# Kernel tuning notes

Hardware: AMD Instinct MI355X
Metric: run time of the kernel (lower is better)

The kernel has to match this reference:

```python
import jax, jax.numpy as jnp
import numpy as np

HEADS = 4
DIM_HEAD = 32
DIM = 256
EPS = 1e-12


def setup_inputs() -> dict:
    key = jax.random.key(0)
    ks = jax.random.split(key, 4)
    b, c, n = 8, DIM, 16384
    hidden = HEADS * DIM_HEAD  # 128
    x = jax.random.normal(ks[0], (b, c, n), dtype=jnp.float32)
    w_qkv = jax.random.normal(ks[1], (hidden * 3, c), dtype=jnp.float32) * (1.0 / np.sqrt(c))
    w_out = jax.random.normal(ks[2], (c, hidden), dtype=jnp.float32) * (1.0 / np.sqrt(hidden))
    b_out = jax.random.normal(ks[3], (c,), dtype=jnp.float32) * 0.01
    g = jnp.ones((1, c, 1), dtype=jnp.float32)
    return {"x": x, "w_qkv": w_qkv, "w_out": w_out, "b_out": b_out, "g": g}


def reference(x, w_qkv, w_out, b_out, g):
    b, c, n = x.shape
    scale = DIM_HEAD ** -0.5
    # to_qkv: Conv1d kernel-size 1, no bias == channel matmul
    qkv = jnp.einsum('oc,bcn->bon', w_qkv, x)  # [b, 3*h*d, n]
    q, k, v = jnp.split(qkv, 3, axis=1)
    def to_heads(t):
        return t.reshape(b, HEADS, DIM_HEAD, n)  # b (h d) n -> b h d n
    q, k, v = to_heads(q), to_heads(k), to_heads(v)
    q = jax.nn.softmax(q, axis=-2) * scale      # softmax over d
    k = jax.nn.softmax(k, axis=-1)              # softmax over n
    context = jnp.einsum('bhdn,bhen->bhde', k, v)  # [b,h,d,e]
    out = jnp.einsum('bhde,bhdn->bhen', context, q)  # [b,h,e,n]
    out = out.reshape(b, HEADS * DIM_HEAD, n)   # b h d n -> b (h d) n
    # to_out Conv1d (kernel 1) with bias
    out = jnp.einsum('oc,bcn->bon', w_out, out) + b_out[None, :, None]
    # RMSNorm: F.normalize over channel dim * g * sqrt(c)
    norm = jnp.sqrt(jnp.sum(out * out, axis=1, keepdims=True))
    out = out / jnp.maximum(norm, EPS) * g * jnp.sqrt(jnp.asarray(c, out.dtype))
    return out
```

## Files before the change

kernel.cpp:

```cpp
#include <hip/hip_runtime.h>
#include <hip/hip_bf16.h>
#include <math.h>

#define B_    8
#define C_    256
#define N_    16384
#define H_    4
#define D_    32
#define HID_  128
#define ROWS_ 384
#define SCALE 0.17677669529663687f

typedef __attribute__((ext_vector_type(8))) short bf16x8;
typedef __attribute__((ext_vector_type(16))) float f32x16;

__device__ __forceinline__ short f2bf(float f) {
    union { __hip_bfloat16 h; short s; } u;
    u.h = __float2bfloat16(f);
    return u.s;
}
__device__ __forceinline__ float bf2f(short s) {
    union { unsigned u; float f; } x;
    x.u = ((unsigned)(unsigned short)s) << 16;
    return x.f;
}

__global__ __launch_bounds__(256) void k_conv(
    const float* __restrict__ wqkv, const float* __restrict__ wout,
    short* __restrict__ wrearr, short* __restrict__ woutb)
{
    int i = blockIdx.x * 256 + threadIdx.x;
    if (i < 12288) {
        int tile = i >> 10;
        int ks   = (i >> 6) & 15;
        int l    = i & 63;
        int row  = tile * 32 + (l & 31);
        int k0   = ks * 16 + (l >> 5) * 8;
        const float* src = wqkv + row * 256 + k0;
        float4 f0 = *(const float4*)(src);
        float4 f1 = *(const float4*)(src + 4);
        short o[8] = {f2bf(f0.x), f2bf(f0.y), f2bf(f0.z), f2bf(f0.w),
                      f2bf(f1.x), f2bf(f1.y), f2bf(f1.z), f2bf(f1.w)};
        *(uint4*)(wrearr + (size_t)i * 8) = *(uint4*)o;
    } else {
        int j = (i - 12288) * 4;
        float4 f = *(const float4*)(wout + j);
        short4 s; s.x = f2bf(f.x); s.y = f2bf(f.y); s.z = f2bf(f.z); s.w = f2bf(f.w);
        *(short4*)(woutb + j) = s;
    }
}

__global__ __launch_bounds__(512, 2) void k_qkv(
    const float* __restrict__ x, const short* __restrict__ wrearr,
    short* __restrict__ qtb, short* __restrict__ part16,
    float* __restrict__ partden)
{
    __shared__ __align__(16) char  img[65536];
    __shared__ __align__(16) float xf[32 * 128];

    const int orig = blockIdx.x;
    const int swz  = (orig & 7) * 128 + (orig >> 3);
    const int b    = swz >> 7;
    const int nwin = swz & 127;
    const int nb   = nwin << 7;
    const int t    = threadIdx.x;
    const int l    = t & 63;
    const int wv   = t >> 6;
    const int h    = wv & 3;
    const int ch   = wv >> 2;
    const int c31  = l & 31;
    const int hf   = l >> 5;

    {
        const float* xg = x + (size_t)b * C_ * N_ + nb + (l & 31) * 4;
        const int cvn  = t & 127;
        const int cvkq = t >> 7;
        const float* xcol = xf + cvn;
        char* imgn = img + cvn * 512;
        const int swm = (cvn & 31) << 4;

        for (int c = 0; c < 8; c++) {
#pragma unroll
            for (int j = 0; j < 2; j++) {
                const int krow = (j * 8 + wv) * 2 + hf;
                const int kglob = c * 32 + krow;
                __builtin_amdgcn_global_load_lds(
                    (const __attribute__((address_space(1))) void*)(xg + (size_t)kglob * N_),
                    (__attribute__((address_space(3))) void*)((char*)xf + (j * 8 + wv) * 1024),
                    16, 0, 0);
            }
            __syncthreads();
#pragma unroll
            for (int p = 0; p < 4; p++) {
                const int kl = cvkq * 8 + p * 2;
                float f0 = xcol[(size_t)kl * 128];
                float f1 = xcol[(size_t)(kl + 1) * 128];
                const int kglob = c * 32 + kl;
                ushort2 v;
                v.x = (unsigned short)f2bf(f0);
                v.y = (unsigned short)f2bf(f1);
                *(ushort2*)(imgn + ((2 * kglob) ^ swm)) = v;
            }
            __syncthreads();
        }
    }

    f32x16 acc[3][2];
#pragma unroll
    for (int ti = 0; ti < 3; ti++)
#pragma unroll
        for (int ct = 0; ct < 2; ct++)
#pragma unroll
            for (int r = 0; r < 16; r++) acc[ti][ct][r] = 0.f;

    const bf16x8* wp = (const bf16x8*)wrearr + (size_t)h * 1024 + l;
    bf16x8 afN0 = wp[0], afN1 = wp[4096], afN2 = wp[8192];
    const char* smB0 = img + (ch * 64 + c31) * 512;
    const char* smB1 = img + (ch * 64 + 32 + c31) * 512;
#pragma unroll
    for (int ks = 0; ks < 16; ks++) {
        bf16x8 af0 = afN0, af1 = afN1, af2 = afN2;
        if (ks < 15) {
            afN0 = wp[(ks + 1) * 64];
            afN1 = wp[4096 + (ks + 1) * 64];
            afN2 = wp[8192 + (ks + 1) * 64];
        }
        const int slot = 2 * ks + hf;
        bf16x8 bfr0 = *(const bf16x8*)(smB0 + 16 * (slot ^ c31));
        bf16x8 bfr1 = *(const bf16x8*)(smB1 + 16 * (slot ^ c31));
        acc[0][0] = __builtin_amdgcn_mfma_f32_32x32x16_bf16(af0, bfr0, acc[0][0], 0, 0, 0);
        acc[0][1] = __builtin_amdgcn_mfma_f32_32x32x16_bf16(af0, bfr1, acc[0][1], 0, 0, 0);
        acc[1][0] = __builtin_amdgcn_mfma_f32_32x32x16_bf16(af1, bfr0, acc[1][0], 0, 0, 0);
        acc[1][1] = __builtin_amdgcn_mfma_f32_32x32x16_bf16(af1, bfr1, acc[1][1], 0, 0, 0);
        acc[2][0] = __builtin_amdgcn_mfma_f32_32x32x16_bf16(af2, bfr0, acc[2][0], 0, 0, 0);
        acc[2][1] = __builtin_amdgcn_mfma_f32_32x32x16_bf16(af2, bfr1, acc[2][1], 0, 0, 0);
    }


#pragma unroll
    for (int ct = 0; ct < 2; ct++) {
        float mx = -1e30f;
#pragma unroll
        for (int r = 0; r < 16; r++) mx = fmaxf(mx, acc[0][ct][r]);
        mx = fmaxf(mx, __shfl_xor(mx, 32));
        float e[16]; float s = 0.f;
#pragma unroll
        for (int r = 0; r < 16; r++) { e[r] = __expf(acc[0][ct][r] - mx); s += e[r]; }
        s += __shfl_xor(s, 32);
        float inv = SCALE / s;
        short* qp = qtb + ((size_t)b * HID_ + h * 32) * N_ + nb + ch * 64 + ct * 32 + c31;
#pragma unroll
        for (int r = 0; r < 16; r++) {
            int rm = (r & 3) + 8 * (r >> 2) + 4 * hf;
            qp[(size_t)rm * N_] = f2bf(e[r] * inv);
        }
    }
    __syncthreads();

    char* ekb = img + wv * 8192;
    char* vvb = ekb + 4096;
#pragma unroll
    for (int ct = 0; ct < 2; ct++)
#pragma unroll
        for (int r = 0; r < 16; r++) {
            int rm = (r & 3) + 8 * (r >> 2) + 4 * hf;
            int n  = ct * 32 + c31;
            int ad = rm * 128 + ((2 * n) ^ ((rm & 7) << 4));
            *(short*)(ekb + ad) = f2bf(__expf(acc[1][ct][r]));
            *(short*)(vvb + ad) = f2bf(acc[2][ct][r]);
        }

    f32x16 cD, dD;
#pragma unroll
    for (int r = 0; r < 16; r++) { cD[r] = 0.f; dD[r] = 0.f; }
    bf16x8 ones;
#pragma unroll
    for (int i = 0; i < 8; i++) ones[i] = (short)0x3F80;
#pragma unroll
    for (int ks = 0; ks < 4; ks++) {
        int slot = 2 * ks + hf;
        bf16x8 ea = *(const bf16x8*)(ekb + c31 * 128 + 16 * (slot ^ (c31 & 7)));
        bf16x8 vb = *(const bf16x8*)(vvb + c31 * 128 + 16 * (slot ^ (c31 & 7)));
        cD = __builtin_amdgcn_mfma_f32_32x32x16_bf16(ea, vb,   cD, 0, 0, 0);
        dD = __builtin_amdgcn_mfma_f32_32x32x16_bf16(ea, ones, dD, 0, 0, 0);
    }

    const int q64 = nwin * 2 + ch;
    short* pb = part16 + ((size_t)(b * 256 + q64) * 4 + h) * 1024;
#pragma unroll
    for (int r = 0; r < 16; r++) {
        int rm = (r & 3) + 8 * (r >> 2) + 4 * hf;
        pb[rm * 32 + c31] = f2bf(cD[r]);
    }
    if (c31 == 0) {
        float* pd = partden + ((size_t)(b * 256 + q64) * 4 + h) * 32;
#pragma unroll
        for (int r = 0; r < 16; r++) {
            int rm = (r & 3) + 8 * (r >> 2) + 4 * hf;
            pd[rm] = dD[r];
        }
    }
}

__global__ __launch_bounds__(256) void k_red(
    const short* __restrict__ part16, const float* __restrict__ partden,
    short* __restrict__ ctxbf)
{
    __shared__ float den_s[32];
    const int bh = blockIdx.x;
    const int b  = bh >> 2, h = bh & 3;
    const int t  = threadIdx.x;
    const int d  = t >> 3;
    const int e4 = (t & 7) * 4;

    const short* p0 = part16 + ((size_t)(b * 256) * 4 + h) * 1024 + d * 32 + e4;
    float s0 = 0.f, s1 = 0.f, s2 = 0.f, s3 = 0.f;
    for (int q = 0; q < 256; q++) {
        short4 v = *(const short4*)(p0 + (size_t)q * 4096);
        s0 += bf2f(v.x); s1 += bf2f(v.y); s2 += bf2f(v.z); s3 += bf2f(v.w);
    }
    if ((t & 7) == 0) {
        const float* pd = partden + ((size_t)(b * 256) * 4 + h) * 32 + d;
        float ds = 0.f;
        for (int q = 0; q < 256; q++) ds += pd[(size_t)q * 128];
        den_s[d] = ds;
    }
    __syncthreads();
    float inv = 1.0f / den_s[d];
    short* cb = ctxbf + (size_t)bh * 1024 + d;
    cb[(e4 + 0) * 32] = f2bf(s0 * inv);
    cb[(e4 + 1) * 32] = f2bf(s1 * inv);
    cb[(e4 + 2) * 32] = f2bf(s2 * inv);
    cb[(e4 + 3) * 32] = f2bf(s3 * inv);
}

__global__ __launch_bounds__(256, 3) void k_out(
    const short* __restrict__ qtb, const short* __restrict__ ctxbf,
    const short* __restrict__ woutb, const float* __restrict__ bout,
    const float* __restrict__ g, float* __restrict__ out)
{
    __shared__ __align__(16) char  hidS[16384];
    __shared__ float gl[C_], bl[C_];
    __shared__ float red[4][64];
    __shared__ float nrm[64];

    const int blk = blockIdx.x;
    const int b   = blk >> 8;
    const int n0  = (blk & 255) << 6;
    const int t   = threadIdx.x;
    const int l   = t & 63;
    const int wv  = t >> 6;
    const int c31 = l & 31;
    const int hf  = l >> 5;

    gl[t] = g[t];
    bl[t] = bout[t];
    __syncthreads();

    f32x16 hD[2];
#pragma unroll
    for (int ct = 0; ct < 2; ct++)
#pragma unroll
        for (int r = 0; r < 16; r++) hD[ct][r] = 0.f;
    const short* qb = qtb + (size_t)b * HID_ * N_ + n0;
    const short* cb = ctxbf + ((size_t)(b * H_ + wv) * 32 + c31) * 32;
#pragma unroll
    for (int ks = 0; ks < 2; ks++) {
        int k0 = ks * 16 + hf * 8;
        bf16x8 af = *(const bf16x8*)(cb + k0);
#pragma unroll
        for (int ct = 0; ct < 2; ct++) {
            bf16x8 bq;
#pragma unroll
            for (int i = 0; i < 8; i++)
                bq[i] = qb[(size_t)(wv * 32 + k0 + i) * N_ + ct * 32 + c31];
            hD[ct] = __builtin_amdgcn_mfma_f32_32x32x16_bf16(af, bq, hD[ct], 0, 0, 0);
        }
    }
#pragma unroll
    for (int ct = 0; ct < 2; ct++)
#pragma unroll
        for (int r = 0; r < 16; r++) {
            int rm = (r & 3) + 8 * (r >> 2) + 4 * hf;
            int hfull = wv * 32 + rm;
            int n = ct * 32 + c31;
            int ad = n * 256 + ((2 * hfull) ^ ((n & 15) << 4));
            *(short*)(hidS + ad) = f2bf(hD[ct][r]);
        }
    __syncthreads();

    f32x16 yacc[2][2];
#pragma unroll
    for (int rt = 0; rt < 2; rt++)
#pragma unroll
        for (int ct = 0; ct < 2; ct++)
#pragma unroll
            for (int r = 0; r < 16; r++) yacc[rt][ct][r] = 0.f;

#pragma unroll
    for (int ks = 0; ks < 8; ks++) {
        int k0 = ks * 16 + hf * 8;
        int sx = 2 * ks + hf;
        bf16x8 bq0 = *(const bf16x8*)(hidS + (c31)      * 256 + 16 * (sx ^ (c31 & 15)));
        bf16x8 bq1 = *(const bf16x8*)(hidS + (c31 + 32) * 256 + 16 * (sx ^ (c31 & 15)));
#pragma unroll
        for (int rt = 0; rt < 2; rt++) {
            bf16x8 af = *(const bf16x8*)(woutb + (wv * 64 + rt * 32 + c31) * HID_ + k0);
            yacc[rt][0] = __builtin_amdgcn_mfma_f32_32x32x16_bf16(af, bq0, yacc[rt][0], 0, 0, 0);
            yacc[rt][1] = __builtin_amdgcn_mfma_f32_32x32x16_bf16(af, bq1, yacc[rt][1], 0, 0, 0);
        }
    }

#pragma unroll
    for (int rt = 0; rt < 2; rt++)
#pragma unroll
        for (int r = 0; r < 16; r++) {
            int rm = (r & 3) + 8 * (r >> 2) + 4 * hf;
            float bo = bl[wv * 64 + rt * 32 + rm];
            yacc[rt][0][r] += bo;
            yacc[rt][1][r] += bo;
        }
#pragma unroll
    for (int ct = 0; ct < 2; ct++) {
        float s = 0.f;
#pragma unroll
        for (int rt = 0; rt < 2; rt++)
#pragma unroll
            for (int r = 0; r < 16; r++) s = fmaf(yacc[rt][ct][r], yacc[rt][ct][r], s);
        s += __shfl_xor(s, 32);
        if (hf == 0) red[wv][ct * 32 + c31] = s;
    }
    __syncthreads();
    if (t < 64) {
        float S = red[0][t] + red[1][t] + red[2][t] + red[3][t];
        nrm[t] = 16.0f / fmaxf(sqrtf(S), 1e-12f);
    }
    __syncthreads();

    float* ob = out + (size_t)b * C_ * N_ + n0;
#pragma unroll
    for (int rt = 0; rt < 2; rt++)
#pragma unroll
        for (int r = 0; r < 16; r++) {
            int rm = (r & 3) + 8 * (r >> 2) + 4 * hf;
            int c  = wv * 64 + rt * 32 + rm;
            float gc = gl[c];
#pragma unroll
            for (int ct = 0; ct < 2; ct++) {
                int n = ct * 32 + c31;
                __builtin_nontemporal_store(yacc[rt][ct][r] * gc * nrm[n],
                                            &ob[(size_t)c * N_ + n]);
            }
        }
}

extern "C" void kernel_launch(void* const* d_in, const int* in_sizes, int n_in,
                              void* d_out, int out_size, void* d_ws, size_t ws_size,
                              hipStream_t stream)
{
    const float* x    = (const float*)d_in[0];
    const float* wqkv = (const float*)d_in[1];
    const float* wout = (const float*)d_in[2];
    const float* bout = (const float*)d_in[3];
    const float* g    = (const float*)d_in[4];
    float* out = (float*)d_out;

    short* qtb     = (short*)d_ws;
    short* part16  = qtb + (size_t)B_ * N_ * HID_;
    float* partden = (float*)(part16 + (size_t)2048 * 4 * 1024);
    short* ctxbf   = (short*)(partden + (size_t)2048 * 4 * 32);
    short* wrearr  = ctxbf + (size_t)B_ * H_ * 32 * 32;
    short* woutb   = wrearr + (size_t)12288 * 8;

    k_conv<<<80, 256, 0, stream>>>(wqkv, wout, wrearr, woutb);
    k_qkv<<<1024, 512, 0, stream>>>(x, wrearr, qtb, part16, partden);
    k_red<<<B_ * H_, 256, 0, stream>>>(part16, partden, ctxbf);
    k_out<<<B_ * (N_ / 64), 256, 0, stream>>>(qtb, ctxbf, woutb, bout, g, out);
}
```

Before: 134.4 us.

## Pre-transpose x into a swizzled bf16 image in a separate kernel

Adds a kernel that converts x to bf16 and writes it already transposed and swizzled into the output buffer, used as scratch. k_qkv then copies its 64KB tile straight into LDS with direct global-to-LDS loads, which drops the in-kernel fp32 staging buffer and the conversion loop with its eight barrier-separated stages. Freeing that LDS lets the launch bound rise to 4 blocks per SM. The cost is an extra launch and an extra global write and read of a bf16 copy of x (about 64MB round trip).

```diff
diff --git a/kernel.cpp b/kernel.cpp
--- a/kernel.cpp
+++ b/kernel.cpp
@@ -50,13 +50,52 @@
     }
 }
 
-__global__ __launch_bounds__(512, 2) void k_qkv(
-    const float* __restrict__ x, const short* __restrict__ wrearr,
+__global__ __launch_bounds__(256, 4) void k_xT(
+    const float* __restrict__ x, short* __restrict__ ximg)
+{
+    __shared__ float xs[8][1028];
+    const int blk = blockIdx.x;
+    const int b   = blk & 7;
+    const int rest= blk >> 3;
+    const int c0  = (rest & 31) * 8;
+    const int nq  = rest >> 5;
+    const int t   = threadIdx.x;
+    const int rg  = t >> 5;
+    const int l32 = t & 31;
+
+    const float* xb = x + ((size_t)b * C_ + c0) * N_;
+    short* chunkbase = ximg + (size_t)b * 128 * 32768;
+
+    for (int it = 0; it < 4; it++) {
+        const int nt = nq * 4096 + it * 1024;
+#pragma unroll
+        for (int j = 0; j < 8; j++) {
+            float4 v = *(const float4*)(xb + (size_t)rg * N_ + nt + j * 128 + l32 * 4);
+            *(float4*)(&xs[rg][j * 128 + l32 * 4]) = v;
+        }
+        __syncthreads();
+#pragma unroll
+        for (int i = 0; i < 4; i++) {
+            int nl = i * 256 + t;
+            int n  = nt + nl;
+            short o[8];
+#pragma unroll
+            for (int c = 0; c < 8; c++) o[c] = f2bf(xs[c][nl]);
+            size_t ad = (size_t)(n >> 7) * 32768
+                      + (size_t)(n & 127) * 256
+                      + (((c0 * 2) ^ ((n & 31) << 4)) >> 1);
+            *(uint4*)(chunkbase + ad) = *(uint4*)o;
+        }
+        __syncthreads();
+    }
+}
+
+__global__ __launch_bounds__(512, 4) void k_qkv(
+    const short* __restrict__ ximg, const short* __restrict__ wrearr,
     short* __restrict__ qtb, short* __restrict__ part16,
     float* __restrict__ partden)
 {
-    __shared__ __align__(16) char  img[65536];
-    __shared__ __align__(16) float xf[32 * 128];
+    __shared__ __align__(16) char img[65536];
 
     const int orig = blockIdx.x;
     const int swz  = (orig & 7) * 128 + (orig >> 3);
@@ -72,38 +111,17 @@
     const int hf   = l >> 5;
 
     {
-        const float* xg = x + (size_t)b * C_ * N_ + nb + (l & 31) * 4;
-        const int cvn  = t & 127;
-        const int cvkq = t >> 7;
-        const float* xcol = xf + cvn;
-        char* imgn = img + cvn * 512;
-        const int swm = (cvn & 31) << 4;
-
-        for (int c = 0; c < 8; c++) {
-#pragma unroll
-            for (int j = 0; j < 2; j++) {
-                const int krow = (j * 8 + wv) * 2 + hf;
-                const int kglob = c * 32 + krow;
-                __builtin_amdgcn_global_load_lds(
-                    (const __attribute__((address_space(1))) void*)(xg + (size_t)kglob * N_),
-                    (__attribute__((address_space(3))) void*)((char*)xf + (j * 8 + wv) * 1024),
-                    16, 0, 0);
-            }
-            __syncthreads();
-#pragma unroll
-            for (int p = 0; p < 4; p++) {
-                const int kl = cvkq * 8 + p * 2;
-                float f0 = xcol[(size_t)kl * 128];
-                float f1 = xcol[(size_t)(kl + 1) * 128];
-                const int kglob = c * 32 + kl;
-                ushort2 v;
-                v.x = (unsigned short)f2bf(f0);
-                v.y = (unsigned short)f2bf(f1);
-                *(ushort2*)(imgn + ((2 * kglob) ^ swm)) = v;
-            }
-            __syncthreads();
-        }
-    }
+        const char* src = (const char*)ximg + (size_t)swz * 65536;
+#pragma unroll
+        for (int i = 0; i < 8; i++) {
+            const int seg = (wv * 8 + i) * 1024;
+            __builtin_amdgcn_global_load_lds(
+                (const __attribute__((address_space(1))) void*)(src + seg + l * 16),
+                (__attribute__((address_space(3))) void*)(img + seg),
+                16, 0, 0);
+        }
+    }
+    __syncthreads();
 
     f32x16 acc[3][2];
 #pragma unroll
@@ -365,6 +383,8 @@
     const float* g    = (const float*)d_in[4];
     float* out = (float*)d_out;
 
+    short* ximg    = (short*)d_out;
+
     short* qtb     = (short*)d_ws;
     short* part16  = qtb + (size_t)B_ * N_ * HID_;
     float* partden = (float*)(part16 + (size_t)2048 * 4 * 1024);
@@ -373,7 +393,8 @@
     short* woutb   = wrearr + (size_t)12288 * 8;
 
     k_conv<<<80, 256, 0, stream>>>(wqkv, wout, wrearr, woutb);
-    k_qkv<<<1024, 512, 0, stream>>>(x, wrearr, qtb, part16, partden);
+    k_xT<<<1024, 256, 0, stream>>>(x, ximg);
+    k_qkv<<<1024, 512, 0, stream>>>(ximg, wrearr, qtb, part16, partden);
     k_red<<<B_ * H_, 256, 0, stream>>>(part16, partden, ctxbf);
     k_out<<<B_ * (N_ / 64), 256, 0, stream>>>(qtb, ctxbf, woutb, bout, g, out);
 }
```

Result: slower. 465.6 us (+246.3%).
